# Performance work log

Hardware: AMD Instinct MI355X
Metric: run time of the kernel (lower is better)

The kernel has to match this reference:

```python
import jax, jax.numpy as jnp
import numpy as np

EPS = 1e-5


def _conv1x1(h, w, b):
    # 1x1 conv == per-pixel matmul: (b,c,h,w) x (o,c) -> (b,o,h,w)
    return jnp.einsum('bchw,oc->bohw', h, w) + b[None, :, None, None]


def setup_inputs() -> dict:
    key = jax.random.key(0)
    ks = jax.random.split(key, 7)
    B, C, H, W = 4, 512, 64, 64
    s = 0.02
    return {
        'x': jax.random.normal(ks[0], (B, C, H, W), dtype=jnp.float32),
        'wq': jax.random.normal(ks[1], (C, C), dtype=jnp.float32) * s,
        'bq': jax.random.normal(ks[2], (C,), dtype=jnp.float32) * s,
        'wk': jax.random.normal(ks[3], (C, C), dtype=jnp.float32) * s,
        'bk': jax.random.normal(ks[4], (C,), dtype=jnp.float32) * s,
        'wv': jax.random.normal(ks[5], (C, C), dtype=jnp.float32) * s,
        'bv': jax.random.normal(ks[6], (C,), dtype=jnp.float32) * s,
    }


def reference(x, wq, bq, wk, bk, wv, bv):
    B, C, H, W = x.shape
    # InstanceNorm2d (affine=False): normalize over spatial dims per (b, c)
    mu = jnp.mean(x, axis=(2, 3), keepdims=True)
    var = jnp.var(x, axis=(2, 3), keepdims=True)  # biased, matches torch
    h_ = (x - mu) * jax.lax.rsqrt(var + EPS)

    q = _conv1x1(h_, wq, bq).reshape(B, C, H * W)  # (b, c, n)
    k = _conv1x1(h_, wk, bk).reshape(B, C, H * W)
    v = _conv1x1(h_, wv, bv).reshape(B, C, H * W)

    scale = float(int(C)) ** (-0.5)
    attn = jnp.einsum('bcq,bck->bqk', q, k) * scale  # (b, n_q, n_k)
    attn = jax.nn.softmax(attn, axis=-1)
    # torch: bmm(v, attn.permute(0,2,1)) -> A[b,c,q] = sum_k v[b,c,k] * attn[b,q,k]
    A = jnp.einsum('bck,bqk->bcq', v, attn).reshape(B, C, H, W)
    return x + A
```

## Files before the change

### kernel.cpp

```cpp
#include <hip/hip_runtime.h>
#include <hip/hip_bf16.h>
#include <cstdint>

#define B_ 4
#define C_ 512
#define N_ 4096

typedef unsigned short u16;
typedef unsigned char u8;
typedef __bf16 bf16x8 __attribute__((ext_vector_type(8)));
typedef float f32x4 __attribute__((ext_vector_type(4)));

union U16B { uint4 u; bf16x8 v; };

__device__ __forceinline__ bf16x8 ld16g(const u16* p) {
  U16B t; t.u = *(const uint4*)p; return t.v;
}

__device__ __forceinline__ u16 f2bf(float f) {
  uint32_t u = __builtin_bit_cast(uint32_t, f);
  u = (u + 0x7FFFu + ((u >> 16) & 1u)) >> 16;
  return (u16)u;
}
__device__ __forceinline__ float bf2f(u16 h) {
  uint32_t u = ((uint32_t)h) << 16;
  return __builtin_bit_cast(float, u);
}

__device__ __forceinline__ u8 f2fp8(float f) {
  uint32_t u = __builtin_bit_cast(uint32_t, f);
  uint32_t s = (u >> 24) & 0x80u;
  uint32_t a = u & 0x7FFFFFFFu;
  if (a >= 0x43700000u) return (u8)(s | 0x7E);
  if (a < 0x3C800000u) {
    float af = __builtin_bit_cast(float, a);
    int m = (int)(af * 512.0f + 0.5f);
    return (u8)(s | (uint32_t)m);
  }
  uint32_t r = (a + 0x7FFFFu + ((a >> 20) & 1u)) >> 20;
  return (u8)(s | (r - (120u << 3)));
}

typedef const __attribute__((address_space(1))) uint32_t* gas_p;
typedef __attribute__((address_space(3))) uint32_t* las_p;
__device__ __forceinline__ void gld16(const void* g, void* l) {
  __builtin_amdgcn_global_load_lds((gas_p)g, (las_p)l, 16, 0, 0);
}

#define SCEXP 0.06376149809794171f

__global__ __launch_bounds__(256) void cvt_w(const float* __restrict__ w, u16* __restrict__ o) {
  int i = blockIdx.x * 256 + threadIdx.x;
  float4 v = ((const float4*)w)[i];
  ushort4 r;
  r.x = f2bf(v.x); r.y = f2bf(v.y); r.z = f2bf(v.z); r.w = f2bf(v.w);
  ((ushort4*)o)[i] = r;
}

__global__ __launch_bounds__(1024) void pack_bias(const float* __restrict__ bq,
    const float* __restrict__ bk, float* __restrict__ o) {
  int i = threadIdx.x;
  o[i] = (i < 512) ? bq[i] : bk[i - 512];
}

__global__ __launch_bounds__(256) void inorm_stats(const float* __restrict__ x,
    float* __restrict__ mu, float* __restrict__ rstd) {
  int bc = blockIdx.x;
  const float4* p = (const float4*)(x + (size_t)bc * N_);
  float s = 0.f, ss = 0.f;
  for (int i = threadIdx.x; i < N_ / 4; i += 256) {
    float4 v = p[i];
    s  += v.x + v.y + v.z + v.w;
    ss += v.x * v.x + v.y * v.y + v.z * v.z + v.w * v.w;
  }
#pragma unroll
  for (int off = 32; off > 0; off >>= 1) {
    s  += __shfl_down(s, off);
    ss += __shfl_down(ss, off);
  }
  __shared__ float as_[4], ass_[4];
  if ((threadIdx.x & 63) == 0) { as_[threadIdx.x >> 6] = s; ass_[threadIdx.x >> 6] = ss; }
  __syncthreads();
  if (threadIdx.x == 0) {
    float S  = as_[0] + as_[1] + as_[2] + as_[3];
    float SS = ass_[0] + ass_[1] + ass_[2] + ass_[3];
    float m  = S * (1.f / N_);
    float var = SS * (1.f / N_) - m * m;
    mu[bc] = m;
    rstd[bc] = rsqrtf(var + 1e-5f);
  }
}

__global__ __launch_bounds__(256) void norm_transpose(const float* __restrict__ x,
    const float* __restrict__ mu, const float* __restrict__ rstd, u16* __restrict__ hT) {
  __shared__ u16 tile[64][66];
  int b = blockIdx.z, c0 = blockIdx.y * 64, n0 = blockIdx.x * 64;
  int tn = threadIdx.x & 63, t4 = threadIdx.x >> 6;
  const float* xb = x + ((size_t)b * C_ + c0) * N_ + n0;
#pragma unroll
  for (int it = 0; it < 16; ++it) {
    int c = t4 + it * 4;
    float m  = mu[b * C_ + c0 + c];
    float rs = rstd[b * C_ + c0 + c];
    tile[c][tn] = f2bf((xb[(size_t)c * N_ + tn] - m) * rs);
  }
  __syncthreads();
  u16* hTb = hT + ((size_t)b * N_ + n0) * C_ + c0;
#pragma unroll
  for (int it = 0; it < 16; ++it) {
    int n = t4 + it * 4;
    hTb[(size_t)n * C_ + tn] = tile[tn][n];
  }
}

#define EPI_BROW 1
#define EPI_QK8  2

template<int EPI>
__global__ __launch_bounds__(256) void gemm128(
    const u16* __restrict__ A, const u16* __restrict__ B,
    const float* __restrict__ aux, void* __restrict__ Out,
    int klen, int lda, int ldb, int ldo,
    long sAz, long sBz, long sOz)
{
  int z = blockIdx.z;
  const u16* Ab = A + (size_t)z * sAz;
  const u16* Bb = B + (size_t)z * sBz;
  int m0 = blockIdx.x * 128, n0 = blockIdx.y * 128;
  int t = threadIdx.x, w = t >> 6, l = t & 63;
  int wr = w >> 1, wc = w & 1;
  int l16 = l & 15, lg = l >> 4;

  __shared__ char smem[65536];

  int srow = t >> 3;
  int scol = ((t & 7) << 4) ^ ((srow & 7) << 4);
  size_t ldaB = (size_t)lda * 2, ldbB = (size_t)ldb * 2;

  f32x4 acc[4][4] = {};
  int nsteps = klen >> 6;

#define STAGE(step, d) {                                                     \
    size_t kbyte = (size_t)(step) * 128 + scol;                              \
    char* lb = smem + (d) * 32768;                                           \
    _Pragma("unroll")                                                        \
    for (int i = 0; i < 4; ++i) {                                            \
      int row = i * 32 + srow;                                               \
      gld16((const char*)Ab + (size_t)(m0 + row) * ldaB + kbyte,             \
            lb + (size_t)(i * 256 + t) * 16);                                \
      gld16((const char*)Bb + (size_t)(n0 + row) * ldbB + kbyte,             \
            lb + 16384 + (size_t)(i * 256 + t) * 16);                        \
    }                                                                        \
  }

  STAGE(0, 0);
  __syncthreads();
  int cur = 0;
  int sw = (l16 & 7) << 4;
  for (int s = 0; s < nsteps; ++s) {
    if (s + 1 < nsteps) STAGE(s + 1, cur ^ 1);
    const char* Al = smem + cur * 32768;
    const char* Bl = Al + 16384;
#pragma unroll
    for (int kc = 0; kc < 2; ++kc) {
      int cb = (kc * 64 + lg * 16) ^ sw;
      bf16x8 af[4], bf[4];
#pragma unroll
      for (int mf = 0; mf < 4; ++mf)
        af[mf] = *(const bf16x8*)(Al + (wr * 64 + mf * 16 + l16) * 128 + cb);
#pragma unroll
      for (int nf = 0; nf < 4; ++nf)
        bf[nf] = *(const bf16x8*)(Bl + (wc * 64 + nf * 16 + l16) * 128 + cb);
#pragma unroll
      for (int mf = 0; mf < 4; ++mf)
#pragma unroll
        for (int nf = 0; nf < 4; ++nf)
          acc[mf][nf] = __builtin_amdgcn_mfma_f32_16x16x32_bf16(af[mf], bf[nf], acc[mf][nf], 0, 0, 0);
    }
    __syncthreads();
    cur ^= 1;
  }
#undef STAGE

  if constexpr (EPI == EPI_BROW) {
    u16* ob = (u16*)Out + (size_t)z * sOz;
#pragma unroll
    for (int mf = 0; mf < 4; ++mf) {
#pragma unroll
      for (int nf = 0; nf < 4; ++nf) {
        int col = n0 + wc * 64 + nf * 16 + l16;
#pragma unroll
        for (int r = 0; r < 4; ++r) {
          int row = m0 + wr * 64 + mf * 16 + lg * 4 + r;
          float v = acc[mf][nf][r] + aux[row];
          ob[(size_t)row * ldo + col] = f2bf(v);
        }
      }
    }
  } else {
    u8* ob = (u8*)Out + (size_t)z * sOz;
    char* sb = smem;
    float bc[4];
#pragma unroll
    for (int nf = 0; nf < 4; ++nf) bc[nf] = aux[n0 + wc * 64 + nf * 16 + l16];
#pragma unroll
    for (int mf = 0; mf < 4; ++mf) {
#pragma unroll
      for (int nf = 0; nf < 4; ++nf) {
        int cl = wc * 64 + nf * 16 + l16;
        int w6 = cl & 63;
        int clp = (cl & 64) | (((w6 >> 3) & 3) * 16) | (((w6 >> 5) & 1) * 8) | (w6 & 7);
#pragma unroll
        for (int r = 0; r < 4; ++r) {
          int rowl = wr * 64 + mf * 16 + lg * 4 + r;
          sb[rowl * 128 + clp] = (char)f2fp8(acc[mf][nf][r] + bc[nf]);
        }
      }
    }
    __syncthreads();
#pragma unroll
    for (int it = 0; it < 4; ++it) {
      int idx = it * 256 + t;
      int row = idx >> 3, seg = idx & 7;
      *(uint4*)(ob + (size_t)(m0 + row) * ldo + n0 + seg * 16) =
          *(const uint4*)(sb + row * 128 + seg * 16);
    }
  }
}

#define STG32(Ab, Bb, ldab, step, lb) {                                      \
    size_t kb = (size_t)(step) * 64;                                         \
    _Pragma("unroll")                                                        \
    for (int i = 0; i < 2; ++i) {                                            \
      int s2 = i * 256 + t;                                                  \
      int row = s2 >> 2;                                                     \
      int sc = (((s2 & 3) ^ ((row >> 1) & 3)) & 3) << 4;                     \
      gld16((const char*)(Ab) + (size_t)(m0 + row) * (ldab) + kb + sc,       \
            (lb) + (size_t)s2 * 16);                                         \
      gld16((const char*)(Bb) + (size_t)(n0 + row) * (ldab) + kb + sc,       \
            (lb) + 8192 + (size_t)s2 * 16);                                  \
    }                                                                        \
  }

#define COMP32(lb) {                                                         \
    const char* Al = (lb);                                                   \
    const char* Bl = (lb) + 8192;                                            \
    bf16x8 af[4], bf[4];                                                     \
    _Pragma("unroll")                                                        \
    for (int mf = 0; mf < 4; ++mf)                                           \
      af[mf] = *(const bf16x8*)(Al + (wr * 64 + mf * 16 + l16) * 64 + rg);   \
    _Pragma("unroll")                                                        \
    for (int nf = 0; nf < 4; ++nf)                                           \
      bf[nf] = *(const bf16x8*)(Bl + (wc * 64 + nf * 16 + l16) * 64 + rg);   \
    _Pragma("unroll")                                                        \
    for (int mf = 0; mf < 4; ++mf)                                           \
      _Pragma("unroll")                                                      \
      for (int nf = 0; nf < 4; ++nf)                                         \
        acc[mf][nf] = __builtin_amdgcn_mfma_f32_16x16x32_bf16(af[mf], bf[nf], acc[mf][nf], 0, 0, 0); \
  }

__global__ __launch_bounds__(512, 2) void exp8(
    const u8* __restrict__ qk8, float* __restrict__ dsumAll, u16* __restrict__ Pall)
{
  int fid = blockIdx.x;
  int rid = (fid & 7) * 256 + (fid >> 3);
  int z = rid >> 9;
  int r9 = rid & 511;
  int c2 = r9 >> 8;
  int r8 = r9 & 255;
  int sm = r8 >> 6, w6s = r8 & 63;
  int m0 = (c2 * 16 + (sm >> 1) * 8 + (w6s >> 3)) * 128;
  int n0 = ((sm & 1) * 8 + (w6s & 7)) * 256;

  const u8* Ab = qk8 + (size_t)z * ((size_t)N_ * 1024);
  const u8* Bb = Ab + 512;
  float* dsum = dsumAll + (size_t)z * N_;
  u16* Pp = Pall + (size_t)z * (size_t)N_ * N_;

  int t = threadIdx.x, w = t >> 6, l = t & 63;
  int wr = w >> 2, wc = w & 3;
  int l16 = l & 15, lg = l >> 4;

  __shared__ char smem[65536];

  f32x4 acc[4][4] = {};
  int rg = ((lg ^ ((l16 >> 1) & 3)) & 3) << 4;

#define STG8(step, lb) {                                                     \
    size_t kb = (size_t)(step) * 64;                                         \
    {                                                                        \
      int row = t >> 2, g = t & 3;                                           \
      int sg = (g ^ ((row >> 1) & 3)) << 4;                                  \
      gld16((const char*)Ab + (size_t)(m0 + row) * 1024 + kb + sg,           \
            (lb) + (size_t)t * 16);                                          \
    }                                                                        \
    _Pragma("unroll")                                                        \
    for (int i = 0; i < 2; ++i) {                                            \
      int s2 = i * 512 + t;                                                  \
      int row = s2 >> 2, g = s2 & 3;                                         \
      int sg = (g ^ ((row >> 1) & 3)) << 4;                                  \
      gld16((const char*)Bb + (size_t)(n0 + row) * 1024 + kb + sg,           \
            (lb) + 8192 + (size_t)s2 * 16);                                  \
    }                                                                        \
  }

#define COMP8(lb) {                                                          \
    const char* Al = (lb);                                                   \
    const char* Bl = (lb) + 8192;                                            \
    uint4 af[4], bf[4];                                                      \
    _Pragma("unroll")                                                        \
    for (int mf = 0; mf < 4; ++mf)                                           \
      af[mf] = *(const uint4*)(Al + (wr * 64 + mf * 16 + l16) * 64 + rg);    \
    _Pragma("unroll")                                                        \
    for (int nf = 0; nf < 4; ++nf)                                           \
      bf[nf] = *(const uint4*)(Bl + (wc * 64 + nf * 16 + l16) * 64 + rg);    \
    _Pragma("unroll")                                                        \
    for (int kk = 0; kk < 2; ++kk) {                                         \
      _Pragma("unroll")                                                      \
      for (int mf = 0; mf < 4; ++mf) {                                       \
        long long a8 = ((long long)(kk ? af[mf].w : af[mf].y) << 32) |       \
                       (unsigned int)(kk ? af[mf].z : af[mf].x);             \
        _Pragma("unroll")                                                    \
        for (int nf = 0; nf < 4; ++nf) {                                     \
          long long b8 = ((long long)(kk ? bf[nf].w : bf[nf].y) << 32) |     \
                         (unsigned int)(kk ? bf[nf].z : bf[nf].x);           \
          acc[mf][nf] = __builtin_amdgcn_mfma_f32_16x16x32_fp8_fp8(          \
              a8, b8, acc[mf][nf], 0, 0, 0);                                 \
        }                                                                    \
      }                                                                      \
    }                                                                        \
  }

  char* buf0 = smem;
  char* buf1 = smem + 24576;

  STG8(0, buf0);
#pragma unroll
  for (int s = 0; s < 8; ++s) {
    char* cb = (s & 1) ? buf1 : buf0;
    char* nb = (s & 1) ? buf0 : buf1;
    if (s < 7) {
      STG8(s + 1, nb);
      asm volatile("s_waitcnt vmcnt(3)" ::: "memory");
    } else {
      asm volatile("s_waitcnt vmcnt(0)" ::: "memory");
    }
    __builtin_amdgcn_s_barrier();
    __builtin_amdgcn_sched_barrier(0);
    COMP8(cb);
    __builtin_amdgcn_sched_barrier(0);
    __builtin_amdgcn_s_barrier();
  }
#undef STG8
#undef COMP8

#pragma unroll
  for (int mf = 0; mf < 4; ++mf) {
#pragma unroll
    for (int r = 0; r < 4; ++r) {
      int row = wr * 64 + mf * 16 + lg * 4 + r;
      int swz = ((row >> 2) & 3) << 5;
      float rs = 0.f;
#pragma unroll
      for (int nf = 0; nf < 4; ++nf) {
        int colb = wc * 128 + nf * 32 + l16 * 2;
        float p = __builtin_amdgcn_exp2f(acc[mf][nf][r] * SCEXP);
        u16 pb = f2bf(p);
        *(u16*)(smem + row * 512 + (colb ^ swz)) = pb;
        rs += bf2f(pb);
      }
      rs += __shfl_xor(rs, 1); rs += __shfl_xor(rs, 2);
      rs += __shfl_xor(rs, 4); rs += __shfl_xor(rs, 8);
      if (l16 == 0) atomicAdd(&dsum[m0 + row], rs);
    }
  }
  __syncthreads();
#pragma unroll
  for (int it = 0; it < 8; ++it) {
    int idx = it * 512 + t;
    int row = idx >> 5, g = idx & 31;
    uint4 v = *(const uint4*)(smem + row * 512 + ((g * 16) ^ (((row >> 2) & 3) << 5)));
    *(uint4*)(Pp + ((size_t)(m0 + row) * N_ + n0 + g * 8)) = v;
  }
}

__global__ __launch_bounds__(256, 3) void pv128(
    const u16* __restrict__ vM, const u16* __restrict__ P,
    const float* __restrict__ denom, const float* __restrict__ x,
    float* __restrict__ out)
{
  int fid = blockIdx.x;
  int rid = (fid & 7) * 64 + (fid >> 3);
  int z = rid >> 7;
  int r7 = rid & 127;
  int n0 = (r7 >> 2) * 128;
  int m0 = (r7 & 3) * 128;

  const u16* Ab = vM + (size_t)z * ((size_t)C_ * N_);
  const u16* Bb = P + (size_t)z * ((size_t)N_ * N_);
  const float* db = denom + (size_t)z * N_;
  const float* xb = x + (size_t)z * ((size_t)C_ * N_);
  float* ob = out + (size_t)z * ((size_t)C_ * N_);

  int t = threadIdx.x, w = t >> 6, l = t & 63;
  int wr = w >> 1, wc = w & 1;
  int l16 = l & 15, lg = l >> 4;

  __shared__ char smem[49152];

  f32x4 acc[4][4] = {};
  int rg = ((lg ^ ((l16 >> 1) & 3)) & 3) << 4;

  char* buf0 = smem;
  char* buf1 = smem + 16384;
  char* buf2 = smem + 32768;

  STG32(Ab, Bb, 8192, 0, buf0);
  STG32(Ab, Bb, 8192, 1, buf1);
#pragma unroll 3
  for (int s = 0; s < 127; ++s) {
    asm volatile("s_waitcnt vmcnt(4)" ::: "memory");
    __builtin_amdgcn_s_barrier();
    __builtin_amdgcn_sched_barrier(0);
    if (s + 2 < 128) STG32(Ab, Bb, 8192, s + 2, buf2);
    COMP32(buf0);
    char* tmp = buf0; buf0 = buf1; buf1 = buf2; buf2 = tmp;
  }
  asm volatile("s_waitcnt vmcnt(0)" ::: "memory");
  __builtin_amdgcn_s_barrier();
  __builtin_amdgcn_sched_barrier(0);
  COMP32(buf0);

  float rd[4];
#pragma unroll
  for (int nf = 0; nf < 4; ++nf)
    rd[nf] = 1.0f / db[n0 + wc * 64 + nf * 16 + l16];
#pragma unroll
  for (int mf = 0; mf < 4; ++mf) {
#pragma unroll
    for (int r = 0; r < 4; ++r) {
      int row = m0 + wr * 64 + mf * 16 + lg * 4 + r;
#pragma unroll
      for (int nf = 0; nf < 4; ++nf) {
        int col = n0 + wc * 64 + nf * 16 + l16;
        size_t o = (size_t)row * N_ + col;
        ob[o] = xb[o] + acc[mf][nf][r] * rd[nf];
      }
    }
  }
}

__global__ __launch_bounds__(256) void gemm_abT(
    const u16* __restrict__ A, const u16* __restrict__ Bm,
    const float* __restrict__ bias, u16* __restrict__ out,
    int ldo, int bias_is_row)
{
  int w = threadIdx.x >> 6, l = threadIdx.x & 63;
  int l16 = l & 15, lg = l >> 4;
  int m0 = blockIdx.x * 128 + (w >> 1) * 64;
  int n0 = blockIdx.y * 128 + (w & 1) * 64;
  f32x4 acc[4][4] = {};
  const u16* Ab = A  + (size_t)(m0 + l16) * 512 + lg * 8;
  const u16* Bb = Bm + (size_t)(n0 + l16) * 512 + lg * 8;
  for (int kc = 0; kc < 512; kc += 32) {
    bf16x8 af[4], bf[4];
#pragma unroll
    for (int i = 0; i < 4; ++i) af[i] = ld16g(Ab + (size_t)(i * 16) * 512 + kc);
#pragma unroll
    for (int j = 0; j < 4; ++j) bf[j] = ld16g(Bb + (size_t)(j * 16) * 512 + kc);
#pragma unroll
    for (int i = 0; i < 4; ++i)
#pragma unroll
      for (int j = 0; j < 4; ++j)
        acc[i][j] = __builtin_amdgcn_mfma_f32_16x16x32_bf16(af[i], bf[j], acc[i][j], 0, 0, 0);
  }
#pragma unroll
  for (int i = 0; i < 4; ++i) {
#pragma unroll
    for (int j = 0; j < 4; ++j) {
      int col = n0 + j * 16 + l16;
#pragma unroll
      for (int r = 0; r < 4; ++r) {
        int row = m0 + i * 16 + lg * 4 + r;
        float v = acc[i][j][r] + (bias_is_row ? bias[row] : bias[col]);
        out[(size_t)row * ldo + col] = f2bf(v);
      }
    }
  }
}

#define NQ 32
#define NKB 64
__global__ __launch_bounds__(512) void attn_kernel(
    const u16* __restrict__ qT, const u16* __restrict__ kT, const u16* __restrict__ vM,
    const float* __restrict__ x, float* __restrict__ out)
{
  int b = blockIdx.y;
  int nq0 = blockIdx.x * NQ;
  const u16* qTb = qT + (size_t)b * N_ * C_;
  const u16* kTb = kT + (size_t)b * N_ * C_;
  const u16* vb  = vM + (size_t)b * C_ * N_;
  const float* xb = x + (size_t)b * C_ * N_;
  float* ob = out + (size_t)b * C_ * N_;

  int tid = threadIdx.x;
  int w = tid >> 6, l = tid & 63, l16 = l & 15, lg = l >> 4;
  int nqf = w & 1, nkf = w >> 1;
  int c0 = w * 64;

  __shared__ u16 qlds[32][520];
  __shared__ u16 Plds[32][72];
  __shared__ float dpart[32][16];
  __shared__ float dfin[32];

  for (int idx = tid; idx < 32 * 64; idx += 512) {
    int row = idx >> 6, cg = idx & 63;
    *(uint4*)&qlds[row][cg * 8] = *(const uint4*)(qTb + (size_t)(nq0 + row) * C_ + cg * 8);
  }
  __syncthreads();

  f32x4 acc[2][4] = {};
  float dreg = 0.f;
  int drow = tid >> 4, dcol = (tid & 15) * 4;

  for (int nk0 = 0; nk0 < N_; nk0 += NKB) {
    f32x4 s = {0.f, 0.f, 0.f, 0.f};
    const u16* krow = kTb + (size_t)(nk0 + nkf * 16 + l16) * C_ + lg * 8;
#pragma unroll 4
    for (int kc = 0; kc < 16; ++kc) {
      U16B tq; tq.u = *(const uint4*)&qlds[nqf * 16 + l16][kc * 32 + lg * 8];
      bf16x8 kf = ld16g(krow + kc * 32);
      s = __builtin_amdgcn_mfma_f32_16x16x32_bf16(tq.v, kf, s, 0, 0, 0);
    }
    __syncthreads();
#pragma unroll
    for (int r = 0; r < 4; ++r) {
      float p = __builtin_amdgcn_exp2f(s[r] * SCEXP);
      Plds[nqf * 16 + lg * 4 + r][nkf * 16 + l16] = f2bf(p);
    }
    __syncthreads();
#pragma unroll
    for (int r = 0; r < 4; ++r) dreg += bf2f(Plds[drow][dcol + r]);
#pragma unroll
    for (int kk = 0; kk < 2; ++kk) {
      bf16x8 pf[2];
#pragma unroll
      for (int i = 0; i < 2; ++i) {
        U16B t2; t2.u = *(const uint4*)&Plds[i * 16 + l16][kk * 32 + lg * 8];
        pf[i] = t2.v;
      }
#pragma unroll
      for (int j = 0; j < 4; ++j) {
        bf16x8 vf = ld16g(vb + (size_t)(c0 + j * 16 + l16) * N_ + nk0 + kk * 32 + lg * 8);
#pragma unroll
        for (int i = 0; i < 2; ++i)
          acc[i][j] = __builtin_amdgcn_mfma_f32_16x16x32_bf16(pf[i], vf, acc[i][j], 0, 0, 0);
      }
    }
  }

  dpart[drow][tid & 15] = dreg;
  __syncthreads();
  if (tid < 32) {
    float s2 = 0.f;
#pragma unroll
    for (int g = 0; g < 16; ++g) s2 += dpart[tid][g];
    dfin[tid] = s2;
  }
  __syncthreads();

#pragma unroll
  for (int i = 0; i < 2; ++i) {
    float dinv[4];
#pragma unroll
    for (int r = 0; r < 4; ++r) dinv[r] = 1.f / dfin[i * 16 + lg * 4 + r];
    int nbase = nq0 + i * 16 + lg * 4;
#pragma unroll
    for (int j = 0; j < 4; ++j) {
      int c = c0 + j * 16 + l16;
      float4 xv = *(const float4*)(xb + (size_t)c * N_ + nbase);
      float4 o;
      o.x = xv.x + acc[i][j][0] * dinv[0];
      o.y = xv.y + acc[i][j][1] * dinv[1];
      o.z = xv.z + acc[i][j][2] * dinv[2];
      o.w = xv.w + acc[i][j][3] * dinv[3];
      *(float4*)(ob + (size_t)c * N_ + nbase) = o;
    }
  }
}

extern "C" void kernel_launch(void* const* d_in, const int* in_sizes, int n_in,
                              void* d_out, int out_size, void* d_ws, size_t ws_size,
                              hipStream_t stream) {
  (void)in_sizes; (void)n_in; (void)out_size;
  const float* x  = (const float*)d_in[0];
  const float* wq = (const float*)d_in[1];
  const float* bq = (const float*)d_in[2];
  const float* wk = (const float*)d_in[3];
  const float* bk = (const float*)d_in[4];
  const float* wv = (const float*)d_in[5];
  const float* bv = (const float*)d_in[6];
  float* out = (float*)d_out;
  char* ws = (char*)d_ws;

  const size_t NC = (size_t)N_ * C_;
  const size_t NEED = 203489280;

  if (ws_size >= NEED) {
    u16*   wbf_q = (u16*)(ws);
    u16*   wbf_k = (u16*)(ws + 524288);
    u16*   wbf_v = (u16*)(ws + 1048576);
    float* bqk   = (float*)(ws + 1572864);
    float* mu    = (float*)(ws + 1581056);
    float* rstd  = (float*)(ws + 1589248);
    u16*   hT    = (u16*)(ws + 1597440);
    u8*    qk8   = (u8*)(ws + 18874368);
    u16*   vM    = (u16*)(ws + 52428800);
    float* denom = (float*)(ws + 69206016);
    u16*   P     = (u16*)(ws + 69271552);

    cvt_w<<<256, 256, 0, stream>>>(wq, wbf_q);
    cvt_w<<<256, 256, 0, stream>>>(wk, wbf_k);
    cvt_w<<<256, 256, 0, stream>>>(wv, wbf_v);
    pack_bias<<<1, 1024, 0, stream>>>(bq, bk, bqk);
    inorm_stats<<<B_ * C_, 256, 0, stream>>>(x, mu, rstd);
    norm_transpose<<<dim3(N_ / 64, C_ / 64, B_), 256, 0, stream>>>(x, mu, rstd, hT);
    hipMemsetAsync(denom, 0, 4 * N_ * sizeof(float), stream);

    gemm128<EPI_QK8><<<dim3(32, 8, 4), 256, 0, stream>>>(
        hT, wbf_q, bqk, qk8, 512, 512, 512, 1024, (long)NC, 0, (long)N_ * 1024);
    gemm128<EPI_BROW><<<dim3(4, 32, 4), 256, 0, stream>>>(
        wbf_v, hT, bv, vM, 512, 512, 512, 4096, 0, (long)NC, (long)NC);

    exp8<<<2048, 512, 0, stream>>>(qk8, denom, P);

    pv128<<<512, 256, 0, stream>>>(vM, P, denom, x, out);
  } else {
    u16*   wbf_q = (u16*)(ws);
    u16*   wbf_k = (u16*)(ws + 524288);
    u16*   wbf_v = (u16*)(ws + 1048576);
    float* mu    = (float*)(ws + 1572864);
    float* rstd  = (float*)(ws + 1581056);
    u16*   hT    = (u16*)(ws + 1589248);
    u16*   qT    = (u16*)(ws + 18366464);
    u16*   kT    = (u16*)(ws + 35143680);
    u16*   vM    = (u16*)(ws + 51920896);

    cvt_w<<<256, 256, 0, stream>>>(wq, wbf_q);
    cvt_w<<<256, 256, 0, stream>>>(wk, wbf_k);
    cvt_w<<<256, 256, 0, stream>>>(wv, wbf_v);
    inorm_stats<<<B_ * C_, 256, 0, stream>>>(x, mu, rstd);
    norm_transpose<<<dim3(N_ / 64, C_ / 64, B_), 256, 0, stream>>>(x, mu, rstd, hT);

    for (int b = 0; b < B_; ++b) {
      const u16* hTb = hT + (size_t)b * NC;
      u16* qTb = qT + (size_t)b * NC;
      u16* kTb = kT + (size_t)b * NC;
      u16* vMb = vM + (size_t)b * NC;
      gemm_abT<<<dim3(N_ / 128, C_ / 128), 256, 0, stream>>>(hTb, wbf_q, bq, qTb, C_, 0);
      gemm_abT<<<dim3(N_ / 128, C_ / 128), 256, 0, stream>>>(hTb, wbf_k, bk, kTb, C_, 0);
      gemm_abT<<<dim3(C_ / 128, N_ / 128), 256, 0, stream>>>(wbf_v, hTb, bv, vMb, N_, 1);
    }
    attn_kernel<<<dim3(N_ / NQ, B_), 512, 0, stream>>>(qT, kT, vM, x, out);
  }
}
```

Measured before the change: 233.9 us.

## Store V and softmax probabilities in fp8 and run PV GEMM with fp8 MFMA

The V projection epilogue now writes fp8 instead of bf16, and the exp kernel writes unnormalized probabilities P as fp8 with row sums taken from the unrounded fp32 values. The final PV GEMM becomes an fp8×fp8 MFMA kernel with double buffering. This halves the dominant N×N P traffic and the V traffic, cutting shared memory so more blocks fit per CU. The cost is reduced accuracy from fp8 quantization of probabilities and values, and denominators no longer match the quantized P exactly.

```diff
diff --git a/kernel.cpp b/kernel.cpp
--- a/kernel.cpp
+++ b/kernel.cpp
@@ -113,8 +113,8 @@
   }
 }
 
-#define EPI_BROW 1
 #define EPI_QK8  2
+#define EPI_V8   3
 
 template<int EPI>
 __global__ __launch_bounds__(256) void gemm128(
@@ -182,85 +182,41 @@
   }
 #undef STAGE
 
-  if constexpr (EPI == EPI_BROW) {
-    u16* ob = (u16*)Out + (size_t)z * sOz;
-#pragma unroll
-    for (int mf = 0; mf < 4; ++mf) {
-#pragma unroll
-      for (int nf = 0; nf < 4; ++nf) {
-        int col = n0 + wc * 64 + nf * 16 + l16;
-#pragma unroll
-        for (int r = 0; r < 4; ++r) {
-          int row = m0 + wr * 64 + mf * 16 + lg * 4 + r;
-          float v = acc[mf][nf][r] + aux[row];
-          ob[(size_t)row * ldo + col] = f2bf(v);
-        }
-      }
-    }
-  } else {
-    u8* ob = (u8*)Out + (size_t)z * sOz;
-    char* sb = smem;
-    float bc[4];
+  u8* ob = (u8*)Out + (size_t)z * sOz;
+  char* sb = smem;
+  float bc[4];
+  if constexpr (EPI == EPI_QK8) {
 #pragma unroll
     for (int nf = 0; nf < 4; ++nf) bc[nf] = aux[n0 + wc * 64 + nf * 16 + l16];
-#pragma unroll
-    for (int mf = 0; mf < 4; ++mf) {
+  }
+#pragma unroll
+  for (int mf = 0; mf < 4; ++mf) {
+#pragma unroll
+    for (int r = 0; r < 4; ++r) {
+      int rowl = wr * 64 + mf * 16 + lg * 4 + r;
+      float brow = (EPI == EPI_V8) ? aux[m0 + rowl] : 0.f;
 #pragma unroll
       for (int nf = 0; nf < 4; ++nf) {
         int cl = wc * 64 + nf * 16 + l16;
         int w6 = cl & 63;
         int clp = (cl & 64) | (((w6 >> 3) & 3) * 16) | (((w6 >> 5) & 1) * 8) | (w6 & 7);
-#pragma unroll
-        for (int r = 0; r < 4; ++r) {
-          int rowl = wr * 64 + mf * 16 + lg * 4 + r;
-          sb[rowl * 128 + clp] = (char)f2fp8(acc[mf][nf][r] + bc[nf]);
-        }
+        float v = acc[mf][nf][r] + (EPI == EPI_QK8 ? bc[nf] : brow);
+        sb[rowl * 128 + clp] = (char)f2fp8(v);
       }
     }
-    __syncthreads();
-#pragma unroll
-    for (int it = 0; it < 4; ++it) {
-      int idx = it * 256 + t;
-      int row = idx >> 3, seg = idx & 7;
-      *(uint4*)(ob + (size_t)(m0 + row) * ldo + n0 + seg * 16) =
-          *(const uint4*)(sb + row * 128 + seg * 16);
-    }
-  }
-}
-
-#define STG32(Ab, Bb, ldab, step, lb) {                                      \
-    size_t kb = (size_t)(step) * 64;                                         \
-    _Pragma("unroll")                                                        \
-    for (int i = 0; i < 2; ++i) {                                            \
-      int s2 = i * 256 + t;                                                  \
-      int row = s2 >> 2;                                                     \
-      int sc = (((s2 & 3) ^ ((row >> 1) & 3)) & 3) << 4;                     \
-      gld16((const char*)(Ab) + (size_t)(m0 + row) * (ldab) + kb + sc,       \
-            (lb) + (size_t)s2 * 16);                                         \
-      gld16((const char*)(Bb) + (size_t)(n0 + row) * (ldab) + kb + sc,       \
-            (lb) + 8192 + (size_t)s2 * 16);                                  \
-    }                                                                        \
-  }
-
-#define COMP32(lb) {                                                         \
-    const char* Al = (lb);                                                   \
-    const char* Bl = (lb) + 8192;                                            \
-    bf16x8 af[4], bf[4];                                                     \
-    _Pragma("unroll")                                                        \
-    for (int mf = 0; mf < 4; ++mf)                                           \
-      af[mf] = *(const bf16x8*)(Al + (wr * 64 + mf * 16 + l16) * 64 + rg);   \
-    _Pragma("unroll")                                                        \
-    for (int nf = 0; nf < 4; ++nf)                                           \
-      bf[nf] = *(const bf16x8*)(Bl + (wc * 64 + nf * 16 + l16) * 64 + rg);   \
-    _Pragma("unroll")                                                        \
-    for (int mf = 0; mf < 4; ++mf)                                           \
-      _Pragma("unroll")                                                      \
-      for (int nf = 0; nf < 4; ++nf)                                         \
-        acc[mf][nf] = __builtin_amdgcn_mfma_f32_16x16x32_bf16(af[mf], bf[nf], acc[mf][nf], 0, 0, 0); \
-  }
-
-__global__ __launch_bounds__(512, 2) void exp8(
-    const u8* __restrict__ qk8, float* __restrict__ dsumAll, u16* __restrict__ Pall)
+  }
+  __syncthreads();
+#pragma unroll
+  for (int it = 0; it < 4; ++it) {
+    int idx = it * 256 + t;
+    int row = idx >> 3, seg = idx & 7;
+    *(uint4*)(ob + (size_t)(m0 + row) * ldo + n0 + seg * 16) =
+        *(const uint4*)(sb + row * 128 + seg * 16);
+  }
+}
+
+__global__ __launch_bounds__(512, 6) void exp8(
+    const u8* __restrict__ qk8, float* __restrict__ dsumAll, u8* __restrict__ Pall)
 {
   int fid = blockIdx.x;
   int rid = (fid & 7) * 256 + (fid >> 3);
@@ -275,13 +231,13 @@
   const u8* Ab = qk8 + (size_t)z * ((size_t)N_ * 1024);
   const u8* Bb = Ab + 512;
   float* dsum = dsumAll + (size_t)z * N_;
-  u16* Pp = Pall + (size_t)z * (size_t)N_ * N_;
+  u8* Pp = Pall + (size_t)z * (size_t)N_ * N_;
 
   int t = threadIdx.x, w = t >> 6, l = t & 63;
   int wr = w >> 2, wc = w & 3;
   int l16 = l & 15, lg = l >> 4;
 
-  __shared__ char smem[65536];
+  __shared__ char smem[49152];
 
   f32x4 acc[4][4] = {};
   int rg = ((lg ^ ((l16 >> 1) & 3)) & 3) << 4;
@@ -359,15 +315,15 @@
 #pragma unroll
     for (int r = 0; r < 4; ++r) {
       int row = wr * 64 + mf * 16 + lg * 4 + r;
-      int swz = ((row >> 2) & 3) << 5;
       float rs = 0.f;
 #pragma unroll
       for (int nf = 0; nf < 4; ++nf) {
-        int colb = wc * 128 + nf * 32 + l16 * 2;
+        int cl = wc * 64 + nf * 16 + l16;
+        int w6 = cl & 63;
+        int clp = (cl & 192) | (((w6 >> 3) & 3) * 16) | (((w6 >> 5) & 1) * 8) | (w6 & 7);
         float p = __builtin_amdgcn_exp2f(acc[mf][nf][r] * SCEXP);
-        u16 pb = f2bf(p);
-        *(u16*)(smem + row * 512 + (colb ^ swz)) = pb;
-        rs += bf2f(pb);
+        rs += p;
+        smem[row * 256 + clp] = (char)f2fp8(p);
       }
       rs += __shfl_xor(rs, 1); rs += __shfl_xor(rs, 2);
       rs += __shfl_xor(rs, 4); rs += __shfl_xor(rs, 8);
@@ -376,16 +332,16 @@
   }
   __syncthreads();
 #pragma unroll
-  for (int it = 0; it < 8; ++it) {
+  for (int it = 0; it < 4; ++it) {
     int idx = it * 512 + t;
-    int row = idx >> 5, g = idx & 31;
-    uint4 v = *(const uint4*)(smem + row * 512 + ((g * 16) ^ (((row >> 2) & 3) << 5)));
-    *(uint4*)(Pp + ((size_t)(m0 + row) * N_ + n0 + g * 8)) = v;
-  }
-}
-
-__global__ __launch_bounds__(256, 3) void pv128(
-    const u16* __restrict__ vM, const u16* __restrict__ P,
+    int row = idx >> 4, seg = idx & 15;
+    *(uint4*)(Pp + ((size_t)(m0 + row) * N_ + n0 + seg * 16)) =
+        *(const uint4*)(smem + row * 256 + seg * 16);
+  }
+}
+
+__global__ __launch_bounds__(256, 4) void pv8(
+    const u8* __restrict__ vM8, const u8* __restrict__ P8,
     const float* __restrict__ denom, const float* __restrict__ x,
     float* __restrict__ out)
 {
@@ -396,8 +352,8 @@
   int n0 = (r7 >> 2) * 128;
   int m0 = (r7 & 3) * 128;
 
-  const u16* Ab = vM + (size_t)z * ((size_t)C_ * N_);
-  const u16* Bb = P + (size_t)z * ((size_t)N_ * N_);
+  const u8* Ab = vM8 + (size_t)z * ((size_t)C_ * N_);
+  const u8* Bb = P8 + (size_t)z * ((size_t)N_ * N_);
   const float* db = denom + (size_t)z * N_;
   const float* xb = x + (size_t)z * ((size_t)C_ * N_);
   float* ob = out + (size_t)z * ((size_t)C_ * N_);
@@ -406,30 +362,74 @@
   int wr = w >> 1, wc = w & 1;
   int l16 = l & 15, lg = l >> 4;
 
-  __shared__ char smem[49152];
+  __shared__ char smem[32768];
 
   f32x4 acc[4][4] = {};
   int rg = ((lg ^ ((l16 >> 1) & 3)) & 3) << 4;
 
+#define STGP(step, lb) {                                                     \
+    size_t kb = (size_t)(step) * 64;                                         \
+    _Pragma("unroll")                                                        \
+    for (int i = 0; i < 2; ++i) {                                            \
+      int s2 = i * 256 + t;                                                  \
+      int row = s2 >> 2, g = s2 & 3;                                         \
+      int sg = (g ^ ((row >> 1) & 3)) << 4;                                  \
+      gld16((const char*)Ab + (size_t)(m0 + row) * N_ + kb + sg,             \
+            (lb) + (size_t)s2 * 16);                                         \
+      gld16((const char*)Bb + (size_t)(n0 + row) * N_ + kb + sg,             \
+            (lb) + 8192 + (size_t)s2 * 16);                                  \
+    }                                                                        \
+  }
+
+#define COMPP(lb) {                                                          \
+    const char* Al = (lb);                                                   \
+    const char* Bl = (lb) + 8192;                                            \
+    uint4 af[4], bf[4];                                                      \
+    _Pragma("unroll")                                                        \
+    for (int mf = 0; mf < 4; ++mf)                                           \
+      af[mf] = *(const uint4*)(Al + (wr * 64 + mf * 16 + l16) * 64 + rg);    \
+    _Pragma("unroll")                                                        \
+    for (int nf = 0; nf < 4; ++nf)                                           \
+      bf[nf] = *(const uint4*)(Bl + (wc * 64 + nf * 16 + l16) * 64 + rg);    \
+    _Pragma("unroll")                                                        \
+    for (int kk = 0; kk < 2; ++kk) {                                         \
+      _Pragma("unroll")                                                      \
+      for (int mf = 0; mf < 4; ++mf) {                                       \
+        long long a8 = ((long long)(kk ? af[mf].w : af[mf].y) << 32) |       \
+                       (unsigned int)(kk ? af[mf].z : af[mf].x);             \
+        _Pragma("unroll")                                                    \
+        for (int nf = 0; nf < 4; ++nf) {                                     \
+          long long b8 = ((long long)(kk ? bf[nf].w : bf[nf].y) << 32) |     \
+                         (unsigned int)(kk ? bf[nf].z : bf[nf].x);           \
+          acc[mf][nf] = __builtin_amdgcn_mfma_f32_16x16x32_fp8_fp8(          \
+              a8, b8, acc[mf][nf], 0, 0, 0);                                 \
+        }                                                                    \
+      }                                                                      \
+    }                                                                        \
+  }
+
   char* buf0 = smem;
   char* buf1 = smem + 16384;
-  char* buf2 = smem + 32768;
-
-  STG32(Ab, Bb, 8192, 0, buf0);
-  STG32(Ab, Bb, 8192, 1, buf1);
-#pragma unroll 3
-  for (int s = 0; s < 127; ++s) {
-    asm volatile("s_waitcnt vmcnt(4)" ::: "memory");
+
+  STGP(0, buf0);
+#pragma unroll 2
+  for (int s = 0; s < 64; ++s) {
+    char* cb = (s & 1) ? buf1 : buf0;
+    char* nb = (s & 1) ? buf0 : buf1;
+    if (s < 63) {
+      STGP(s + 1, nb);
+      asm volatile("s_waitcnt vmcnt(4)" ::: "memory");
+    } else {
+      asm volatile("s_waitcnt vmcnt(0)" ::: "memory");
+    }
     __builtin_amdgcn_s_barrier();
     __builtin_amdgcn_sched_barrier(0);
-    if (s + 2 < 128) STG32(Ab, Bb, 8192, s + 2, buf2);
-    COMP32(buf0);
-    char* tmp = buf0; buf0 = buf1; buf1 = buf2; buf2 = tmp;
-  }
-  asm volatile("s_waitcnt vmcnt(0)" ::: "memory");
-  __builtin_amdgcn_s_barrier();
-  __builtin_amdgcn_sched_barrier(0);
-  COMP32(buf0);
+    COMPP(cb);
+    __builtin_amdgcn_sched_barrier(0);
+    __builtin_amdgcn_s_barrier();
+  }
+#undef STGP
+#undef COMPP
 
   float rd[4];
 #pragma unroll
@@ -604,7 +604,7 @@
   char* ws = (char*)d_ws;
 
   const size_t NC = (size_t)N_ * C_;
-  const size_t NEED = 203489280;
+  const size_t NEED = 136380416;
 
   if (ws_size >= NEED) {
     u16*   wbf_q = (u16*)(ws);
@@ -615,9 +615,9 @@
     float* rstd  = (float*)(ws + 1589248);
     u16*   hT    = (u16*)(ws + 1597440);
     u8*    qk8   = (u8*)(ws + 18874368);
-    u16*   vM    = (u16*)(ws + 52428800);
+    u8*    vM8   = (u8*)(ws + 52428800);
     float* denom = (float*)(ws + 69206016);
-    u16*   P     = (u16*)(ws + 69271552);
+    u8*    P8    = (u8*)(ws + 69271552);
 
     cvt_w<<<256, 256, 0, stream>>>(wq, wbf_q);
     cvt_w<<<256, 256, 0, stream>>>(wk, wbf_k);
@@ -629,12 +629,12 @@
 
     gemm128<EPI_QK8><<<dim3(32, 8, 4), 256, 0, stream>>>(
         hT, wbf_q, bqk, qk8, 512, 512, 512, 1024, (long)NC, 0, (long)N_ * 1024);
-    gemm128<EPI_BROW><<<dim3(4, 32, 4), 256, 0, stream>>>(
-        wbf_v, hT, bv, vM, 512, 512, 512, 4096, 0, (long)NC, (long)NC);
-
-    exp8<<<2048, 512, 0, stream>>>(qk8, denom, P);
-
-    pv128<<<512, 256, 0, stream>>>(vM, P, denom, x, out);
+    gemm128<EPI_V8><<<dim3(4, 32, 4), 256, 0, stream>>>(
+        wbf_v, hT, bv, vM8, 512, 512, 512, 4096, 0, (long)NC, (long)NC);
+
+    exp8<<<2048, 512, 0, stream>>>(qk8, denom, P8);
+
+    pv8<<<512, 256, 0, stream>>>(vM8, P8, denom, x, out);
   } else {
     u16*   wbf_q = (u16*)(ws);
     u16*   wbf_k = (u16*)(ws + 524288);
```

Measured after the change: 446.0 us. 90.7% more time.
